# Kernel optimization log

Hardware: AMD Instinct MI355X
Metric: run time of the kernel (lower is better)

Reference implementation:

```python
import jax, jax.numpy as jnp
import numpy as np

GAMMA = 0.96875
SCALE_BASE = 512.0


def _fixed_pos_embedding(scale):
    # scale: (L, d) where d = head_dim // 2
    L, d = scale.shape
    inv_freq = 1.0 / (10000.0 ** (jnp.arange(d, dtype=jnp.float32) / d))
    sinusoid = jnp.arange(L, dtype=jnp.float32)[:, None] * inv_freq  # (L, d)
    return jnp.sin(sinusoid), jnp.cos(sinusoid)


def _rotate_every_two(x):
    # (..., D) -> (..., D) with pairs (x0, x1) -> (-x1, x0)
    x1 = x[..., ::2]
    x2 = x[..., 1::2]
    return jnp.stack((-x2, x1), axis=-1).reshape(x.shape)


def _dup_interleave(m):
    # (L, d) -> (L, 2d), each column duplicated (matches rotary pairing)
    return jnp.repeat(m, 2, axis=-1)


def xpos(x, offset=0, downscale=False):
    # x: (B, S, D). Standard torchscale-style XPos rotary embedding.
    S, D = x.shape[-2], x.shape[-1]
    scale_vec = (jnp.arange(0, D, 2, dtype=jnp.float32) + 0.4 * D) / (1.4 * D)  # (D/2,)
    min_pos = -(S + offset) // 2
    max_pos = S + offset + min_pos
    power = jnp.arange(min_pos, max_pos, dtype=jnp.float32) / SCALE_BASE  # (S+offset,)
    scale = scale_vec ** power[:, None]  # (S+offset, D/2)
    sin, cos = _fixed_pos_embedding(scale)
    if scale.shape[0] > S:  # keep the last S positions
        scale, sin, cos = scale[-S:], sin[-S:], cos[-S:]
    if downscale:
        scale = 1.0 / scale
    sin = _dup_interleave(sin * scale)  # (S, D)
    cos = _dup_interleave(cos * scale)  # (S, D)
    return x * cos + _rotate_every_two(x) * sin


def _decay_mask(S, dtype):
    # D[n, m] = gamma^(n-m) if n >= m else 0  (lower triangular)
    m = jnp.arange(S)
    diff = m[:, None] - m  # (S, S)
    causal = diff >= 0
    exp = jnp.where(causal, diff, 0).astype(dtype)
    return jnp.where(causal, jnp.asarray(GAMMA, dtype) ** exp, jnp.zeros((), dtype))


def setup_inputs() -> dict:
    key = jax.random.key(0)
    kx, kq, kk, kv = jax.random.split(key, 4)
    B, S, H, Dh = 4, 4096, 2048, 256
    return {
        "x": jax.random.normal(kx, (B, S, H), dtype=jnp.float32),
        "w_q": jax.random.normal(kq, (H, Dh), dtype=jnp.float32),
        "w_k": jax.random.normal(kk, (H, Dh), dtype=jnp.float32),
        "w_v": jax.random.normal(kv, (H, Dh), dtype=jnp.float32),
    }


def reference(x, w_q, w_k, w_v):
    # x: (B, S, H) -> out: (B, S, Dh)
    B, S, _ = x.shape
    decay = _decay_mask(S, x.dtype)[None]  # (1, S, S)
    q = xpos(x @ w_q)                       # (B, S, Dh)
    k = xpos(x @ w_k, downscale=True)       # (B, S, Dh)
    v = x @ w_v                             # (B, S, Dh)
    ret = jnp.einsum("bsd,btd->bst", q, k) * decay  # (B, S, S)
    return jnp.einsum("bst,btd->bsd", ret, v)       # (B, S, Dh)
```

## Files before the change

### kernel.cpp

```cpp
#include <hip/hip_runtime.h>
#include <cstddef>
#include <cstdint>

#define Bn 4
#define Sn 4096
#define Hn 2048
#define Dn 256

typedef float f32x16 __attribute__((ext_vector_type(16)));
typedef short bf16x8 __attribute__((ext_vector_type(8)));

#define AS3 __attribute__((address_space(3)))
#define AS1 __attribute__((address_space(1)))

#define L2G -0.045803689613125f
#define GC 2.9526131e-4f

__device__ __forceinline__ unsigned short f2bf(float f) {
  union { float f; unsigned int u; } a; a.f = f;
  unsigned int r = a.u + 0x7fffu + ((a.u >> 16) & 1u);
  return (unsigned short)(r >> 16);
}
__device__ __forceinline__ float bf2f(unsigned int b) {
  union { unsigned int u; float f; } a; a.u = b << 16;
  return a.f;
}

__global__ __launch_bounds__(256) void prep_kernel(const float* __restrict__ wq,
                                                   const float* __restrict__ wk,
                                                   const float* __restrict__ wv,
                                                   unsigned short* __restrict__ wt,
                                                   float* __restrict__ rt) {
  __shared__ __align__(16) unsigned short T[64][72];
  const int bx = blockIdx.x;
  const int tid = threadIdx.x;
  if (bx < 2048) {
    const int g = bx * 256 + tid;
    const int s = g >> 7;
    const int jp = g & 127;
    const float invf = exp2f((float)jp * (-13.287712379549449f / 128.0f));
    float sn, cs;
    sincosf((float)s * invf, &sn, &cs);
    const float l2sv = log2f((2.0f * jp + 102.4f) * (1.0f / 358.4f));
    const float pw = ((float)s - 2048.0f) * (1.0f / 512.0f);
    const float tl = (float)(s & 255) * L2G;
    const float ex = pw * l2sv + tl;
    const float eq = exp2f(ex), ek = exp2f(-ex);
    float2* q = (float2*)rt;
    float2* k = (float2*)(rt + 4096 * 256);
    q[(size_t)s * 128 + jp] = make_float2(cs * eq, sn * eq);
    k[(size_t)s * 128 + jp] = make_float2(cs * ek, sn * ek);
  } else {
    const int bw = bx - 2048;
    const int k0 = (bw & 31) * 64;
    const int n0 = (bw >> 5) * 64;
    const float* w = (n0 < 256) ? wq : (n0 < 512 ? wk : wv);
    const int nc0 = n0 & 255;
#pragma unroll
    for (int it = 0; it < 2; ++it) {
      int flat = it * 256 + tid;
      int r = flat >> 3, c8 = flat & 7;
      const float* src = w + (size_t)(k0 + r) * 256 + nc0 + c8 * 8;
      float4 v0 = *(const float4*)src;
      float4 v1 = *(const float4*)(src + 4);
      T[c8 * 8 + 0][r] = f2bf(v0.x); T[c8 * 8 + 1][r] = f2bf(v0.y);
      T[c8 * 8 + 2][r] = f2bf(v0.z); T[c8 * 8 + 3][r] = f2bf(v0.w);
      T[c8 * 8 + 4][r] = f2bf(v1.x); T[c8 * 8 + 5][r] = f2bf(v1.y);
      T[c8 * 8 + 6][r] = f2bf(v1.z); T[c8 * 8 + 7][r] = f2bf(v1.w);
    }
    __syncthreads();
#pragma unroll
    for (int it = 0; it < 2; ++it) {
      int flat = it * 256 + tid;
      int nr = flat >> 3, kc8 = flat & 7;
      int n = n0 + nr;
      int kc_sw = kc8 ^ (n & 7);
      uint4 val = *(const uint4*)&T[nr][kc8 * 8];
      *(uint4*)((char*)wt + (size_t)n * 4096 + (size_t)k0 * 2 + kc_sw * 16) = val;
    }
  }
}

__global__ __launch_bounds__(256, 2) void proj9_kernel(const float* __restrict__ x,
                                                       const unsigned short* __restrict__ wt,
                                                       const float* __restrict__ rt,
                                                       unsigned short* __restrict__ qkv,
                                                       unsigned short* __restrict__ kt,
                                                       unsigned short* __restrict__ vt) {
  __shared__ __align__(16) char smem[40960];
  unsigned short* As = (unsigned short*)smem;
  const int tid = threadIdx.x;
  const int lane = tid & 63;
  const int wc = tid >> 6;
  const int m0 = blockIdx.x * 64;
  const int kind = blockIdx.y;
  const int l31 = lane & 31, lh = lane >> 5;

  const int arow = tid >> 2;
  const int acg = (tid & 3) << 4;
  const int asw = (arow & 7) << 4;

  f32x16 acc[2][2];
#pragma unroll
  for (int i = 0; i < 2; ++i)
#pragma unroll
    for (int j = 0; j < 2; ++j) acc[i][j] = 0.0f;

  for (int k0 = 0; k0 < Hn; k0 += 64) {
    const float* srcA = x + (size_t)(m0 + arow) * 2048 + k0 + acg;
    float4 f0 = ((const float4*)srcA)[0];
    float4 f1 = ((const float4*)srcA)[1];
    float4 f2 = ((const float4*)srcA)[2];
    float4 f3 = ((const float4*)srcA)[3];
    {
      AS3 char* ldsb = (AS3 char*)(smem + 8192);
#pragma unroll
      for (int i = 0; i < 8; ++i) {
        int ou = i * 4096 + wc * 1024;
        int o = ou + lane * 16;
        int row = o >> 7, colB = o & 127;
        const char* srcB = (const char*)wt + (size_t)(kind * 256 + row) * 4096 + k0 * 2 + colB;
        __builtin_amdgcn_global_load_lds((const AS1 unsigned int*)srcB,
                                         (AS3 unsigned int*)(ldsb + ou), 16, 0, 0);
      }
    }
    {
      uint4 u0, u1;
      asm("v_cvt_pk_bf16_f32 %0, %1, %2" : "=v"(u0.x) : "v"(f0.x), "v"(f0.y));
      asm("v_cvt_pk_bf16_f32 %0, %1, %2" : "=v"(u0.y) : "v"(f0.z), "v"(f0.w));
      asm("v_cvt_pk_bf16_f32 %0, %1, %2" : "=v"(u0.z) : "v"(f1.x), "v"(f1.y));
      asm("v_cvt_pk_bf16_f32 %0, %1, %2" : "=v"(u0.w) : "v"(f1.z), "v"(f1.w));
      asm("v_cvt_pk_bf16_f32 %0, %1, %2" : "=v"(u1.x) : "v"(f2.x), "v"(f2.y));
      asm("v_cvt_pk_bf16_f32 %0, %1, %2" : "=v"(u1.y) : "v"(f2.z), "v"(f2.w));
      asm("v_cvt_pk_bf16_f32 %0, %1, %2" : "=v"(u1.z) : "v"(f3.x), "v"(f3.y));
      asm("v_cvt_pk_bf16_f32 %0, %1, %2" : "=v"(u1.w) : "v"(f3.z), "v"(f3.w));
      *(uint4*)((char*)As + arow * 128 + ((acg * 2) ^ asw)) = u0;
      *(uint4*)((char*)As + arow * 128 + ((acg * 2 + 16) ^ asw)) = u1;
    }
    __syncthreads();
#pragma unroll
    for (int kc = 0; kc < 4; ++kc) {
      const int kb = kc * 32 + lh * 16;
      bf16x8 a[2], b[2];
#pragma unroll
      for (int i = 0; i < 2; ++i) {
        int mr = i * 32 + l31;
        a[i] = *(const bf16x8*)((const char*)As + mr * 128 + (kb ^ ((mr & 7) << 4)));
        int nr = wc * 64 + i * 32 + l31;
        b[i] = *(const bf16x8*)(smem + 8192 + nr * 128 + (kb ^ ((nr & 7) << 4)));
      }
#pragma unroll
      for (int i = 0; i < 2; ++i)
#pragma unroll
        for (int j = 0; j < 2; ++j)
          acc[i][j] = __builtin_amdgcn_mfma_f32_32x32x16_bf16(a[i], b[j], acc[i][j], 0, 0, 0);
    }
    __syncthreads();
  }

  const int bidx = m0 >> 12;
  const int t0b = m0 & 4095;

  if (kind < 2) {
    const float* rtb = rt + (size_t)kind * (4096 * 256);
    int jp[2];
#pragma unroll
    for (int j = 0; j < 2; ++j) jp[j] = (wc * 64 + j * 32 + l31) >> 1;
    const int odd = l31 & 1;
#pragma unroll
    for (int i = 0; i < 2; ++i)
#pragma unroll
      for (int reg = 0; reg < 16; ++reg) {
        const int mm = m0 + i * 32 + (reg & 3) + 8 * (reg >> 2) + 4 * lh;
        const int s = mm & (Sn - 1);
#pragma unroll
        for (int j = 0; j < 2; ++j) {
          const float2 cf = *(const float2*)(rtb + (size_t)s * 256 + jp[j] * 2);
          float v = acc[i][j][reg];
          float p = __shfl_xor(v, 1, 64);
          acc[i][j][reg] = odd ? (v * cf.x + p * cf.y) : (v * cf.x - p * cf.y);
        }
      }
  }

  if (kind == 0) {
#pragma unroll
    for (int i = 0; i < 2; ++i)
#pragma unroll
      for (int j = 0; j < 2; ++j)
#pragma unroll
        for (int reg = 0; reg < 16; ++reg) {
          int m = m0 + i * 32 + (reg & 3) + 8 * (reg >> 2) + 4 * lh;
          int n = wc * 64 + j * 32 + l31;
          qkv[(size_t)m * 768 + n] = f2bf(acc[i][j][reg]);
        }
  } else {
    if (kind == 1) {
#pragma unroll
      for (int i = 0; i < 2; ++i)
#pragma unroll
        for (int j = 0; j < 2; ++j)
#pragma unroll
          for (int reg = 0; reg < 16; ++reg) {
            int m = m0 + i * 32 + (reg & 3) + 8 * (reg >> 2) + 4 * lh;
            int d = wc * 64 + j * 32 + l31;
            qkv[(size_t)m * 768 + 256 + (d ^ ((m & 7) << 3))] = f2bf(acc[i][j][reg]);
          }
    }
    unsigned short* dst = (kind == 1) ? kt : vt;
#pragma unroll
    for (int h = 0; h < 2; ++h) {
      __syncthreads();
      if ((wc >> 1) == h) {
#pragma unroll
        for (int i = 0; i < 2; ++i)
#pragma unroll
          for (int j = 0; j < 2; ++j) {
            const int dl = (wc & 1) * 64 + j * 32 + l31;
#pragma unroll
            for (int k8 = 0; k8 < 8; ++k8) {
              const int r0 = 2 * k8;
              const int t = i * 32 + (r0 & 3) + 8 * (r0 >> 2) + 4 * lh;
              unsigned int pk;
              asm("v_cvt_pk_bf16_f32 %0, %1, %2" : "=v"(pk)
                  : "v"(acc[i][j][r0]), "v"(acc[i][j][r0 + 1]));
              *(unsigned int*)(smem + dl * 128 + ((2 * t) ^ ((dl & 7) << 4))) = pk;
            }
          }
      }
      __syncthreads();
#pragma unroll
      for (int p = 0; p < 4; ++p) {
        const int fl = p * 256 + tid;
        const int dl = fl >> 3, t8 = fl & 7;
        uint4 val = *(const uint4*)(smem + dl * 128 + ((t8 * 16) ^ ((dl & 7) << 4)));
        *(uint4*)(dst + (size_t)(bidx * 256 + h * 128 + dl) * 4096 + t0b + t8 * 8) = val;
      }
    }
  }
}

__global__ __launch_bounds__(256) void wt_build(const float* __restrict__ wq,
                                                const float* __restrict__ wk,
                                                const float* __restrict__ wv,
                                                unsigned short* __restrict__ wt) {
  __shared__ __align__(16) unsigned short T[64][72];
  const int tid = threadIdx.x;
  const int k0 = blockIdx.x * 64;
  const int n0 = blockIdx.y * 64;
  const float* w = (n0 < 256) ? wq : (n0 < 512 ? wk : wv);
  const int nc0 = n0 & 255;
#pragma unroll
  for (int it = 0; it < 2; ++it) {
    int flat = it * 256 + tid;
    int r = flat >> 3, c8 = flat & 7;
    const float* src = w + (size_t)(k0 + r) * 256 + nc0 + c8 * 8;
    float4 v0 = *(const float4*)src;
    float4 v1 = *(const float4*)(src + 4);
    T[c8 * 8 + 0][r] = f2bf(v0.x); T[c8 * 8 + 1][r] = f2bf(v0.y);
    T[c8 * 8 + 2][r] = f2bf(v0.z); T[c8 * 8 + 3][r] = f2bf(v0.w);
    T[c8 * 8 + 4][r] = f2bf(v1.x); T[c8 * 8 + 5][r] = f2bf(v1.y);
    T[c8 * 8 + 6][r] = f2bf(v1.z); T[c8 * 8 + 7][r] = f2bf(v1.w);
  }
  __syncthreads();
#pragma unroll
  for (int it = 0; it < 2; ++it) {
    int flat = it * 256 + tid;
    int nr = flat >> 3, kc8 = flat & 7;
    int n = n0 + nr;
    int kc_sw = kc8 ^ (n & 7);
    uint4 val = *(const uint4*)&T[nr][kc8 * 8];
    *(uint4*)((char*)wt + (size_t)n * 4096 + (size_t)k0 * 2 + kc_sw * 16) = val;
  }
}

__global__ __launch_bounds__(256, 2) void proj_kernel(const float* __restrict__ x,
                                                      const unsigned short* __restrict__ wt,
                                                      unsigned short* __restrict__ qkv) {
  __shared__ __align__(16) unsigned short As[128 * 64];
  __shared__ __align__(16) unsigned short Bs[128 * 64];
  const int tid = threadIdx.x;
  const int lane = tid & 63;
  const int wid = tid >> 6;
  const int wr = wid >> 1, wc = wid & 1;
  const int m0 = blockIdx.x * 128;
  const int n0 = blockIdx.y * 128;
  const int l31 = lane & 31, lh = lane >> 5;

  f32x16 acc[2][2];
#pragma unroll
  for (int i = 0; i < 2; ++i)
#pragma unroll
    for (int j = 0; j < 2; ++j) acc[i][j] = 0.0f;

  for (int k0 = 0; k0 < Hn; k0 += 64) {
    {
      AS3 char* ldsb = (AS3 char*)Bs;
#pragma unroll
      for (int i = 0; i < 4; ++i) {
        int ou = i * 4096 + wid * 1024;
        int o = ou + lane * 16;
        int row = o >> 7, col = o & 127;
        const char* src = (const char*)wt + (size_t)(n0 + row) * 4096 + k0 * 2 + col;
        __builtin_amdgcn_global_load_lds((const AS1 unsigned int*)src,
                                         (AS3 unsigned int*)(ldsb + ou), 16, 0, 0);
      }
    }
#pragma unroll
    for (int i = 0; i < 4; ++i) {
      int o = i * 256 + tid;
      int row = o >> 3, c8 = o & 7;
      const float* src = x + (size_t)(m0 + row) * 2048 + k0 + c8 * 8;
      float4 v0 = *(const float4*)src;
      float4 v1 = *(const float4*)(src + 4);
      uint4 val;
      val.x = f2bf(v0.x) | ((unsigned int)f2bf(v0.y) << 16);
      val.y = f2bf(v0.z) | ((unsigned int)f2bf(v0.w) << 16);
      val.z = f2bf(v1.x) | ((unsigned int)f2bf(v1.y) << 16);
      val.w = f2bf(v1.z) | ((unsigned int)f2bf(v1.w) << 16);
      *(uint4*)((char*)As + row * 128 + ((c8 * 16) ^ ((row & 7) << 4))) = val;
    }
    __syncthreads();
#pragma unroll
    for (int kc = 0; kc < 4; ++kc) {
      const int kb = kc * 32 + lh * 16;
      bf16x8 a[2], b[2];
#pragma unroll
      for (int i = 0; i < 2; ++i) {
        int mr = wr * 64 + i * 32 + l31;
        a[i] = *(const bf16x8*)((const char*)As + mr * 128 + (kb ^ ((mr & 7) << 4)));
        int nr = wc * 64 + i * 32 + l31;
        b[i] = *(const bf16x8*)((const char*)Bs + nr * 128 + (kb ^ ((nr & 7) << 4)));
      }
#pragma unroll
      for (int i = 0; i < 2; ++i)
#pragma unroll
        for (int j = 0; j < 2; ++j)
          acc[i][j] = __builtin_amdgcn_mfma_f32_32x32x16_bf16(a[i], b[j], acc[i][j], 0, 0, 0);
    }
    __syncthreads();
  }
  const bool khalf = (n0 >= 256 && n0 < 512);
#pragma unroll
  for (int i = 0; i < 2; ++i)
#pragma unroll
    for (int j = 0; j < 2; ++j)
#pragma unroll
      for (int reg = 0; reg < 16; ++reg) {
        int m = m0 + wr * 64 + i * 32 + (reg & 3) + 8 * (reg >> 2) + 4 * lh;
        int n = n0 + wc * 64 + j * 32 + l31;
        if (khalf) n = 256 + ((n - 256) ^ ((m & 7) << 3));
        qkv[(size_t)m * 768 + n] = f2bf(acc[i][j][reg]);
      }
}

__global__ __launch_bounds__(256) void xpos_kernel(unsigned short* __restrict__ qkv) {
  const int g = blockIdx.x * 256 + threadIdx.x;
  const int m = g >> 5;
  const int c = g & 31;
  const float s = (float)(m & (Sn - 1));
  unsigned short* qrow = qkv + (size_t)m * 768;
  const int csw = c ^ (m & 7);
  uint4 qv = *(uint4*)(qrow + c * 8);
  uint4 kv = *(uint4*)(qrow + 256 + csw * 8);
  unsigned int* qu = (unsigned int*)&qv;
  unsigned int* ku = (unsigned int*)&kv;
  const float pw = (s - 2048.0f) * (1.0f / 512.0f);
  const float gp = exp2f((float)(m & 255) * L2G);
#pragma unroll
  for (int p = 0; p < 4; ++p) {
    const int jp = c * 4 + p;
    const float invf = exp2f((float)jp * (-13.287712379549449f / 128.0f));
    float sn, cs;
    sincosf(s * invf, &sn, &cs);
    const float sv = (2.0f * jp + 102.4f) * (1.0f / 358.4f);
    const float scq = exp2f(pw * log2f(sv)) * gp;
    const float sci = 1.0f / scq;
    float q0 = bf2f(qu[p] & 0xffffu), q1 = bf2f(qu[p] >> 16);
    float k0 = bf2f(ku[p] & 0xffffu), k1 = bf2f(ku[p] >> 16);
    float q0r = (q0 * cs - q1 * sn) * scq;
    float q1r = (q1 * cs + q0 * sn) * scq;
    float k0r = (k0 * cs - k1 * sn) * sci;
    float k1r = (k1 * cs + k0 * sn) * sci;
    qu[p] = f2bf(q0r) | ((unsigned int)f2bf(q1r) << 16);
    ku[p] = f2bf(k0r) | ((unsigned int)f2bf(k1r) << 16);
  }
  *(uint4*)(qrow + c * 8) = qv;
  *(uint4*)(qrow + 256 + csw * 8) = kv;
}

__global__ __launch_bounds__(256) void kvt_build(const unsigned short* __restrict__ qkv,
                                                 unsigned short* __restrict__ kt,
                                                 unsigned short* __restrict__ vt) {
  __shared__ __align__(16) unsigned short Tk[64][72];
  __shared__ __align__(16) unsigned short Tv[64][72];
  const int tid = threadIdx.x;
  const int t0 = blockIdx.x * 64;
  const int d0 = blockIdx.y * 64;
  const int b = blockIdx.z;
  const size_t rowb = ((size_t)b * Sn + t0) * 1536;
#pragma unroll
  for (int it = 0; it < 2; ++it) {
    int flat = it * 256 + tid;
    int r = flat >> 3, c8 = flat & 7;
    int kc = (d0 >> 3) + c8;
    int kcs = kc ^ (r & 7);
    uint4 kvv = *(const uint4*)((const char*)qkv + rowb + (size_t)r * 1536 + 512 + kcs * 16);
    uint4 vvv = *(const uint4*)((const char*)qkv + rowb + (size_t)r * 1536 + 1024 + (size_t)(d0 + c8 * 8) * 2);
    const unsigned short* ke = (const unsigned short*)&kvv;
    const unsigned short* ve = (const unsigned short*)&vvv;
#pragma unroll
    for (int e = 0; e < 8; ++e) { Tk[c8 * 8 + e][r] = ke[e]; Tv[c8 * 8 + e][r] = ve[e]; }
  }
  __syncthreads();
#pragma unroll
  for (int it = 0; it < 2; ++it) {
    int flat = it * 256 + tid;
    int dr = flat >> 3, tc8 = flat & 7;
    *(uint4*)(kt + (size_t)(b * 256 + d0 + dr) * 4096 + t0 + tc8 * 8) = *(const uint4*)&Tk[dr][tc8 * 8];
    *(uint4*)(vt + (size_t)(b * 256 + d0 + dr) * 4096 + t0 + tc8 * 8) = *(const uint4*)&Tv[dr][tc8 * 8];
  }
}

__global__ __launch_bounds__(256) void mbuild_kernel(const unsigned short* __restrict__ kt,
                                                     const unsigned short* __restrict__ vt,
                                                     unsigned short* __restrict__ mt) {
  const int tid = threadIdx.x;
  const int lane = tid & 63;
  const int wid = tid >> 6;
  const int l31 = lane & 31, lh = lane >> 5;
  const int jc = blockIdx.x;
  const int quad = blockIdx.y;
  const int b = blockIdx.z;
  const int d2w = ((quad >> 1) * 2 + (wid >> 1)) * 64;
  const int d1w = ((quad & 1) * 2 + (wid & 1)) * 64;
  const size_t tb = (size_t)jc * 256;

  f32x16 acc[2][2];
#pragma unroll
  for (int i = 0; i < 2; ++i)
#pragma unroll
    for (int j = 0; j < 2; ++j) acc[i][j] = 0.0f;

#pragma unroll 2
  for (int dc = 0; dc < 16; ++dc) {
    const int ko = dc * 32 + lh * 16;
    bf16x8 a[2], bb[2];
#pragma unroll
    for (int i = 0; i < 2; ++i) {
      a[i]  = *(const bf16x8*)((const char*)vt + ((size_t)(b * 256 + d2w + i * 32 + l31) * 4096 + tb) * 2 + ko);
      bb[i] = *(const bf16x8*)((const char*)kt + ((size_t)(b * 256 + d1w + i * 32 + l31) * 4096 + tb) * 2 + ko);
    }
#pragma unroll
    for (int i = 0; i < 2; ++i)
#pragma unroll
      for (int j = 0; j < 2; ++j)
        acc[i][j] = __builtin_amdgcn_mfma_f32_32x32x16_bf16(a[i], bb[j], acc[i][j], 0, 0, 0);
  }
  unsigned short* dst = mt + ((size_t)(b * 16 + jc) << 16);
#pragma unroll
  for (int i = 0; i < 2; ++i)
#pragma unroll
    for (int j = 0; j < 2; ++j)
#pragma unroll
      for (int reg = 0; reg < 16; ++reg) {
        int row = d2w + i * 32 + (reg & 3) + 8 * (reg >> 2) + 4 * lh;
        int col = d1w + j * 32 + l31;
        dst[row * 256 + col] = f2bf(acc[i][j][reg]);
      }
}

__global__ __launch_bounds__(256) void scan_kernel(unsigned short* __restrict__ mt) {
  const int e0 = (blockIdx.x * 256 + threadIdx.x) * 4;
  const int b = blockIdx.y;
  unsigned short* base = mt + ((size_t)b << 20);
  float s0 = 0.f, s1 = 0.f, s2 = 0.f, s3 = 0.f;
  for (int j = 1; j < 16; ++j) {
    unsigned short* p = base + ((size_t)(j - 1) << 16) + e0;
    uint2 mv = *(const uint2*)p;
    s0 = GC * (s0 + bf2f(mv.x & 0xffffu));
    s1 = GC * (s1 + bf2f(mv.x >> 16));
    s2 = GC * (s2 + bf2f(mv.y & 0xffffu));
    s3 = GC * (s3 + bf2f(mv.y >> 16));
    uint2 w;
    w.x = f2bf(s0) | ((unsigned int)f2bf(s1) << 16);
    w.y = f2bf(s2) | ((unsigned int)f2bf(s3) << 16);
    *(uint2*)p = w;
  }
}

__global__ __launch_bounds__(256, 2) void retc_kernel(const unsigned short* __restrict__ qkv,
                                                      const unsigned short* __restrict__ vt,
                                                      const unsigned short* __restrict__ mt,
                                                      float* __restrict__ out) {
  __shared__ float cmb[2][32][128];
  const int tid = threadIdx.x;
  const int lane = tid & 63;
  const int tw = tid >> 6;
  const int l31 = lane & 31, lh = lane >> 5;
  const int st = blockIdx.x;
  const int dh = blockIdx.y;
  const int b = blockIdx.z;
  const int j = st >> 3;
  const int base = st & ~7;
  const int s0 = st * 32;
  const int d0 = dh * 128;

  bf16x8 qf[16];
  {
    const char* qrow = (const char*)qkv + ((size_t)b * Sn + s0 + l31) * 1536;
#pragma unroll
    for (int dc = 0; dc < 16; ++dc)
      qf[dc] = *(const bf16x8*)(qrow + dc * 32 + lh * 16);
  }

  f32x16 acc[4];
#pragma unroll
  for (int i = 0; i < 4; ++i) acc[i] = 0.0f;

  if (j > 0) {
    const char* Sj = (const char*)mt + ((size_t)(b * 16 + j - 1) << 17);
#pragma unroll
    for (int dcl = 0; dcl < 4; ++dcl) {
      const int dc = tw * 4 + dcl;
#pragma unroll
      for (int g = 0; g < 4; ++g) {
        const int d2 = d0 + g * 32 + l31;
        bf16x8 sbf = *(const bf16x8*)(Sj + (size_t)d2 * 512 + dc * 32 + lh * 16);
        acc[g] = __builtin_amdgcn_mfma_f32_32x32x16_bf16(qf[dc], sbf, acc[g], 0, 0, 0);
      }
    }
  }

  const int sg = s0 + l31;
  const int ksw = (l31 & 7) << 4;
  for (int tt = base; tt <= st; ++tt) {
    if (((tt - base) & 3) != tw) continue;
    const bool msk = (tt == st);
    const int t0 = tt * 32;

    f32x16 sacc = 0.0f;
    const char* krow = (const char*)qkv + ((size_t)b * Sn + t0 + l31) * 1536 + 512;
    __builtin_amdgcn_s_setprio(1);
#pragma unroll
    for (int dc = 0; dc < 16; ++dc) {
      bf16x8 kf = *(const bf16x8*)(krow + ((dc * 32 + lh * 16) ^ ksw));
      sacc = __builtin_amdgcn_mfma_f32_32x32x16_bf16(kf, qf[dc], sacc, 0, 0, 0);
    }
    __builtin_amdgcn_s_setprio(0);

    unsigned int P[8];
#pragma unroll
    for (int k = 0; k < 8; ++k) {
      const int r0 = 2 * k;
      float f0 = sacc[r0], f1 = sacc[r0 + 1];
      if (msk) {
        const int tg0 = t0 + (r0 & 3) + 8 * (r0 >> 2) + 4 * lh;
        f0 = (sg - tg0 >= 0) ? f0 : 0.0f;
        f1 = (sg - tg0 - 1 >= 0) ? f1 : 0.0f;
      }
      unsigned int pk;
      asm("v_cvt_pk_bf16_f32 %0, %1, %2" : "=v"(pk) : "v"(f0), "v"(f1));
      P[k] = pk;
    }
    asm volatile("v_permlane32_swap_b32 %0, %1" : "+v"(P[0]), "+v"(P[2]));
    asm volatile("v_permlane32_swap_b32 %0, %1" : "+v"(P[1]), "+v"(P[3]));
    asm volatile("v_permlane32_swap_b32 %0, %1" : "+v"(P[4]), "+v"(P[6]));
    asm volatile("v_permlane32_swap_b32 %0, %1" : "+v"(P[5]), "+v"(P[7]));

    __builtin_amdgcn_s_setprio(1);
#pragma unroll
    for (int kc = 0; kc < 2; ++kc) {
      uint4 pw;
      pw.x = P[kc * 4 + 0]; pw.y = P[kc * 4 + 1];
      pw.z = P[kc * 4 + 2]; pw.w = P[kc * 4 + 3];
      bf16x8 pf = *(const bf16x8*)&pw;
#pragma unroll
      for (int g = 0; g < 4; ++g) {
        const int d = d0 + g * 32 + l31;
        bf16x8 vf = *(const bf16x8*)((const char*)vt +
            ((size_t)(b * 256 + d) * 4096 + t0) * 2 + kc * 32 + lh * 16);
        acc[g] = __builtin_amdgcn_mfma_f32_32x32x16_bf16(pf, vf, acc[g], 0, 0, 0);
      }
    }
    __builtin_amdgcn_s_setprio(0);
  }

  if (tw >= 2) {
#pragma unroll
    for (int g = 0; g < 4; ++g)
#pragma unroll
      for (int reg = 0; reg < 16; ++reg) {
        int sl = (reg & 3) + 8 * (reg >> 2) + 4 * lh;
        cmb[tw - 2][sl][g * 32 + l31] = acc[g][reg];
      }
  }
  __syncthreads();
  if (tw < 2) {
#pragma unroll
    for (int g = 0; g < 4; ++g)
#pragma unroll
      for (int reg = 0; reg < 16; ++reg) {
        int sl = (reg & 3) + 8 * (reg >> 2) + 4 * lh;
        acc[g][reg] += cmb[tw][sl][g * 32 + l31];
      }
  }
  __syncthreads();
  if (tw == 1) {
#pragma unroll
    for (int g = 0; g < 4; ++g)
#pragma unroll
      for (int reg = 0; reg < 16; ++reg) {
        int sl = (reg & 3) + 8 * (reg >> 2) + 4 * lh;
        cmb[0][sl][g * 32 + l31] = acc[g][reg];
      }
  }
  __syncthreads();
  if (tw == 0) {
#pragma unroll
    for (int g = 0; g < 4; ++g)
#pragma unroll
      for (int reg = 0; reg < 16; ++reg) {
        int sl = (reg & 3) + 8 * (reg >> 2) + 4 * lh;
        int c = g * 32 + l31;
        out[((size_t)(b * Sn + s0 + sl)) * 256 + d0 + c] = acc[g][reg] + cmb[0][sl][c];
      }
  }
}

extern "C" void kernel_launch(void* const* d_in, const int* in_sizes, int n_in,
                              void* d_out, int out_size, void* d_ws, size_t ws_size,
                              hipStream_t stream) {
  (void)in_sizes; (void)n_in; (void)out_size;
  const float* x  = (const float*)d_in[0];
  const float* wq = (const float*)d_in[1];
  const float* wk = (const float*)d_in[2];
  const float* wv = (const float*)d_in[3];
  float* out = (float*)d_out;
  char* ws = (char*)d_ws;

  unsigned short* qkv = (unsigned short*)(ws);
  unsigned short* vt  = (unsigned short*)(ws + 25165824);
  unsigned short* kt  = (unsigned short*)(ws + 33554432);
  unsigned short* mt  = (unsigned short*)(ws + 41943040);

  const size_t NEED_BIG = 128974848;
  if (ws_size >= NEED_BIG) {
    unsigned short* wt = (unsigned short*)(ws + 117440512);
    float*          rtab = (float*)(ws + 120586240);
    prep_kernel<<<2432, 256, 0, stream>>>(wq, wk, wv, wt, rtab);
    proj9_kernel<<<dim3(256, 3), 256, 0, stream>>>(x, wt, rtab, qkv, kt, vt);
  } else {
    unsigned short* wt = (unsigned short*)(ws + 41943040);
    wt_build<<<dim3(32, 12), 256, 0, stream>>>(wq, wk, wv, wt);
    proj_kernel<<<dim3(128, 6), 256, 0, stream>>>(x, wt, qkv);
    xpos_kernel<<<2048, 256, 0, stream>>>(qkv);
    kvt_build<<<dim3(64, 4, 4), 256, 0, stream>>>(qkv, kt, vt);
  }
  mbuild_kernel<<<dim3(16, 4, 4), 256, 0, stream>>>(kt, vt, mt);
  scan_kernel<<<dim3(64, 4), 256, 0, stream>>>(mt);
  retc_kernel<<<dim3(128, 2, 4), 256, 0, stream>>>(qkv, vt, mt, out);
}
```

Measured before the change: 165.0 us.

## Double-buffer LDS tiles in projection GEMM to overlap loads with MFMA

Restructures the projection kernel's K loop into a two-stage software pipeline. The next tile's x values are loaded into registers and the next weight tile is issued through global_load_lds into a second LDS buffer while MFMAs run on the current buffer. This removes one barrier per iteration and hides global-load latency behind compute. LDS use doubles to 80 KB per block, which may limit the two-blocks-per-CU occupancy and raises register pressure from the prefetched float4s.

```diff
diff --git a/kernel.cpp b/kernel.cpp
--- a/kernel.cpp
+++ b/kernel.cpp
@@ -81,14 +81,13 @@
   }
 }
 
-__global__ __launch_bounds__(256, 2) void proj9_kernel(const float* __restrict__ x,
-                                                       const unsigned short* __restrict__ wt,
-                                                       const float* __restrict__ rt,
-                                                       unsigned short* __restrict__ qkv,
-                                                       unsigned short* __restrict__ kt,
-                                                       unsigned short* __restrict__ vt) {
-  __shared__ __align__(16) char smem[40960];
-  unsigned short* As = (unsigned short*)smem;
+__global__ __launch_bounds__(256, 2) void proj10_kernel(const float* __restrict__ x,
+                                                        const unsigned short* __restrict__ wt,
+                                                        const float* __restrict__ rt,
+                                                        unsigned short* __restrict__ qkv,
+                                                        unsigned short* __restrict__ kt,
+                                                        unsigned short* __restrict__ vt) {
+  __shared__ __align__(16) char smem[81920];
   const int tid = threadIdx.x;
   const int lane = tid & 63;
   const int wc = tid >> 6;
@@ -99,6 +98,7 @@
   const int arow = tid >> 2;
   const int acg = (tid & 3) << 4;
   const int asw = (arow & 7) << 4;
+  const float* arowp = x + (size_t)(m0 + arow) * 2048 + acg;
 
   f32x16 acc[2][2];
 #pragma unroll
@@ -106,12 +106,9 @@
 #pragma unroll
     for (int j = 0; j < 2; ++j) acc[i][j] = 0.0f;
 
-  for (int k0 = 0; k0 < Hn; k0 += 64) {
-    const float* srcA = x + (size_t)(m0 + arow) * 2048 + k0 + acg;
-    float4 f0 = ((const float4*)srcA)[0];
-    float4 f1 = ((const float4*)srcA)[1];
-    float4 f2 = ((const float4*)srcA)[2];
-    float4 f3 = ((const float4*)srcA)[3];
+  {
+    const float4* s = (const float4*)arowp;
+    float4 f0 = s[0], f1 = s[1], f2 = s[2], f3 = s[3];
     {
       AS3 char* ldsb = (AS3 char*)(smem + 8192);
 #pragma unroll
@@ -119,25 +116,45 @@
         int ou = i * 4096 + wc * 1024;
         int o = ou + lane * 16;
         int row = o >> 7, colB = o & 127;
-        const char* srcB = (const char*)wt + (size_t)(kind * 256 + row) * 4096 + k0 * 2 + colB;
+        const char* srcB = (const char*)wt + (size_t)(kind * 256 + row) * 4096 + colB;
         __builtin_amdgcn_global_load_lds((const AS1 unsigned int*)srcB,
                                          (AS3 unsigned int*)(ldsb + ou), 16, 0, 0);
       }
     }
-    {
-      uint4 u0, u1;
-      asm("v_cvt_pk_bf16_f32 %0, %1, %2" : "=v"(u0.x) : "v"(f0.x), "v"(f0.y));
-      asm("v_cvt_pk_bf16_f32 %0, %1, %2" : "=v"(u0.y) : "v"(f0.z), "v"(f0.w));
-      asm("v_cvt_pk_bf16_f32 %0, %1, %2" : "=v"(u0.z) : "v"(f1.x), "v"(f1.y));
-      asm("v_cvt_pk_bf16_f32 %0, %1, %2" : "=v"(u0.w) : "v"(f1.z), "v"(f1.w));
-      asm("v_cvt_pk_bf16_f32 %0, %1, %2" : "=v"(u1.x) : "v"(f2.x), "v"(f2.y));
-      asm("v_cvt_pk_bf16_f32 %0, %1, %2" : "=v"(u1.y) : "v"(f2.z), "v"(f2.w));
-      asm("v_cvt_pk_bf16_f32 %0, %1, %2" : "=v"(u1.z) : "v"(f3.x), "v"(f3.y));
-      asm("v_cvt_pk_bf16_f32 %0, %1, %2" : "=v"(u1.w) : "v"(f3.z), "v"(f3.w));
-      *(uint4*)((char*)As + arow * 128 + ((acg * 2) ^ asw)) = u0;
-      *(uint4*)((char*)As + arow * 128 + ((acg * 2 + 16) ^ asw)) = u1;
-    }
-    __syncthreads();
+    uint4 u0, u1;
+    asm("v_cvt_pk_bf16_f32 %0, %1, %2" : "=v"(u0.x) : "v"(f0.x), "v"(f0.y));
+    asm("v_cvt_pk_bf16_f32 %0, %1, %2" : "=v"(u0.y) : "v"(f0.z), "v"(f0.w));
+    asm("v_cvt_pk_bf16_f32 %0, %1, %2" : "=v"(u0.z) : "v"(f1.x), "v"(f1.y));
+    asm("v_cvt_pk_bf16_f32 %0, %1, %2" : "=v"(u0.w) : "v"(f1.z), "v"(f1.w));
+    asm("v_cvt_pk_bf16_f32 %0, %1, %2" : "=v"(u1.x) : "v"(f2.x), "v"(f2.y));
+    asm("v_cvt_pk_bf16_f32 %0, %1, %2" : "=v"(u1.y) : "v"(f2.z), "v"(f2.w));
+    asm("v_cvt_pk_bf16_f32 %0, %1, %2" : "=v"(u1.z) : "v"(f3.x), "v"(f3.y));
+    asm("v_cvt_pk_bf16_f32 %0, %1, %2" : "=v"(u1.w) : "v"(f3.z), "v"(f3.w));
+    *(uint4*)(smem + arow * 128 + ((acg * 2) ^ asw)) = u0;
+    *(uint4*)(smem + arow * 128 + ((acg * 2 + 16) ^ asw)) = u1;
+  }
+  __syncthreads();
+
+  int buf = 0;
+  for (int t = 0; t < 32; ++t) {
+    const char* cur = smem + buf * 40960;
+    char* nxt = smem + (buf ^ 1) * 40960;
+    float4 n0, n1, n2, n3;
+    if (t < 31) {
+      const float4* s = (const float4*)(arowp + (t + 1) * 64);
+      n0 = s[0]; n1 = s[1]; n2 = s[2]; n3 = s[3];
+      AS3 char* ldsb = (AS3 char*)(nxt + 8192);
+      const int kB = (t + 1) * 128;
+#pragma unroll
+      for (int i = 0; i < 8; ++i) {
+        int ou = i * 4096 + wc * 1024;
+        int o = ou + lane * 16;
+        int row = o >> 7, colB = o & 127;
+        const char* srcB = (const char*)wt + (size_t)(kind * 256 + row) * 4096 + kB + colB;
+        __builtin_amdgcn_global_load_lds((const AS1 unsigned int*)srcB,
+                                         (AS3 unsigned int*)(ldsb + ou), 16, 0, 0);
+      }
+    }
 #pragma unroll
     for (int kc = 0; kc < 4; ++kc) {
       const int kb = kc * 32 + lh * 16;
@@ -145,9 +162,9 @@
 #pragma unroll
       for (int i = 0; i < 2; ++i) {
         int mr = i * 32 + l31;
-        a[i] = *(const bf16x8*)((const char*)As + mr * 128 + (kb ^ ((mr & 7) << 4)));
+        a[i] = *(const bf16x8*)(cur + mr * 128 + (kb ^ ((mr & 7) << 4)));
         int nr = wc * 64 + i * 32 + l31;
-        b[i] = *(const bf16x8*)(smem + 8192 + nr * 128 + (kb ^ ((nr & 7) << 4)));
+        b[i] = *(const bf16x8*)(cur + 8192 + nr * 128 + (kb ^ ((nr & 7) << 4)));
       }
 #pragma unroll
       for (int i = 0; i < 2; ++i)
@@ -155,7 +172,21 @@
         for (int j = 0; j < 2; ++j)
           acc[i][j] = __builtin_amdgcn_mfma_f32_32x32x16_bf16(a[i], b[j], acc[i][j], 0, 0, 0);
     }
+    if (t < 31) {
+      uint4 u0, u1;
+      asm("v_cvt_pk_bf16_f32 %0, %1, %2" : "=v"(u0.x) : "v"(n0.x), "v"(n0.y));
+      asm("v_cvt_pk_bf16_f32 %0, %1, %2" : "=v"(u0.y) : "v"(n0.z), "v"(n0.w));
+      asm("v_cvt_pk_bf16_f32 %0, %1, %2" : "=v"(u0.z) : "v"(n1.x), "v"(n1.y));
+      asm("v_cvt_pk_bf16_f32 %0, %1, %2" : "=v"(u0.w) : "v"(n1.z), "v"(n1.w));
+      asm("v_cvt_pk_bf16_f32 %0, %1, %2" : "=v"(u1.x) : "v"(n2.x), "v"(n2.y));
+      asm("v_cvt_pk_bf16_f32 %0, %1, %2" : "=v"(u1.y) : "v"(n2.z), "v"(n2.w));
+      asm("v_cvt_pk_bf16_f32 %0, %1, %2" : "=v"(u1.z) : "v"(n3.x), "v"(n3.y));
+      asm("v_cvt_pk_bf16_f32 %0, %1, %2" : "=v"(u1.w) : "v"(n3.z), "v"(n3.w));
+      *(uint4*)(nxt + arow * 128 + ((acg * 2) ^ asw)) = u0;
+      *(uint4*)(nxt + arow * 128 + ((acg * 2 + 16) ^ asw)) = u1;
+    }
     __syncthreads();
+    buf ^= 1;
   }
 
   const int bidx = m0 >> 12;
@@ -649,7 +680,7 @@
     unsigned short* wt = (unsigned short*)(ws + 117440512);
     float*          rtab = (float*)(ws + 120586240);
     prep_kernel<<<2432, 256, 0, stream>>>(wq, wk, wv, wt, rtab);
-    proj9_kernel<<<dim3(256, 3), 256, 0, stream>>>(x, wt, rtab, qkv, kt, vt);
+    proj10_kernel<<<dim3(256, 3), 256, 0, stream>>>(x, wt, rtab, qkv, kt, vt);
   } else {
     unsigned short* wt = (unsigned short*)(ws + 41943040);
     wt_build<<<dim3(32, 12), 256, 0, stream>>>(wq, wk, wv, wt);
```

After: 183.2 us. 11.1% more time.
